# Kernel optimization log

Hardware: AMD Instinct MI355X
Metric: run time of the kernel (lower is better)

## Reference

```python
import jax, jax.numpy as jnp
import numpy as np

BIG_K = 13
EPS = 1e-5  # torch BatchNorm2d default


def setup_inputs() -> dict:
    key = jax.random.key(0)
    k1, k2, k3, k4 = jax.random.split(key, 4)
    B, C1, C2, H, W_ = 8, 256, 256, 64, 64
    x = jax.random.normal(k1, (B, C1, H, W_), dtype=jnp.float32)
    # scale kernel by fan-in so pre-BN activations are O(1)
    fan_in = C1 * BIG_K * BIG_K
    W = jax.random.normal(k2, (C2, C1, BIG_K, BIG_K), dtype=jnp.float32) / np.sqrt(fan_in)
    gamma = jnp.ones((C2,), dtype=jnp.float32)
    beta = jnp.zeros((C2,), dtype=jnp.float32)
    running_mean = jax.random.normal(k3, (C2,), dtype=jnp.float32) * 0.1
    running_var = jax.random.uniform(k4, (C2,), dtype=jnp.float32, minval=0.5, maxval=1.5)
    return {"x": x, "W": W, "gamma": gamma, "beta": beta,
            "running_mean": running_mean, "running_var": running_var}


def reference(x, W, gamma, beta, running_mean, running_var):
    # Fallback path of ShiftWiseConv: big-kernel conv (no bias) -> BN (inference) -> SiLU
    pad = BIG_K // 2
    y = jax.lax.conv_general_dilated(
        x, W,
        window_strides=(1, 1),
        padding=[(pad, pad), (pad, pad)],
        dimension_numbers=("NCHW", "OIHW", "NCHW"),
    )
    inv = gamma * jax.lax.rsqrt(running_var + EPS)  # [C2]
    y = y * inv[None, :, None, None] + (beta - running_mean * inv)[None, :, None, None]
    return jax.nn.silu(y)
```

## Files before the change

kernel.cpp:

```cpp
#include <hip/hip_runtime.h>
#include <stdint.h>

#define EPS 1e-5f

typedef __attribute__((ext_vector_type(8))) __bf16 bf16x8;
typedef __attribute__((ext_vector_type(16))) float f32x16;

__device__ __forceinline__ int swz4(int r) { return (r ^ (r >> 2)) & 3; }

__device__ __forceinline__ unsigned short f2bf(float f) {
  union { float f; unsigned u; } v; v.f = f;
  unsigned r = v.u + 0x7fffu + ((v.u >> 16) & 1u);
  return (unsigned short)(r >> 16);
}

__device__ __forceinline__ void glds16(const unsigned short* g, unsigned short* l) {
  __builtin_amdgcn_global_load_lds(
      (const __attribute__((address_space(1))) void*)g,
      (__attribute__((address_space(3))) void*)l, 16, 0, 0);
}
__device__ __forceinline__ void glds4(const unsigned short* g, unsigned short* l) {
  __builtin_amdgcn_global_load_lds(
      (const __attribute__((address_space(1))) void*)g,
      (__attribute__((address_space(3))) void*)l, 4, 0, 0);
}

template <int N>
__device__ __forceinline__ void vmwait() {
  asm volatile("s_waitcnt vmcnt(%0)" ::"n"(N) : "memory");
}

__global__ __launch_bounds__(256) void pack_w_kernel(
    const float* __restrict__ W, unsigned short* __restrict__ Wp) {
  const int blk = blockIdx.x;
  const int c2 = blk / 13, kh = blk - c2 * 13;
  const int c1 = threadIdx.x;
  const int c2t = c2 >> 7, m = c2 & 127;
  const int c1c = c1 >> 5, c1i = c1 & 31;
  const float* src = W + (((size_t)(c2 * 256 + c1)) * 13 + kh) * 13;
  const int rowoff = (((c1i >> 3) ^ swz4(m)) << 3) + (c1i & 7);
#pragma unroll
  for (int kw = 0; kw < 13; ++kw) {
    const int ks = (kh * 8 + c1c) * 13 + kw;
    const size_t dst = (((size_t)c2t * 1352 + ks) * 128 + m) * 32 + rowoff;
    Wp[dst] = f2bf(src[kw]);
  }
}

__global__ __launch_bounds__(256) void pack_xt_kernel(
    const float* __restrict__ x, unsigned short* __restrict__ xT) {
  const int blk = blockIdx.x;
  const int rowp = blk % 76;
  const int bc = blk / 76;
  const int c1c = bc & 7, b = bc >> 3;
  const int row = rowp - 6;
  const bool rok = (unsigned)row < 64u;
  unsigned short* dst = xT + (size_t)blk * 2560;
  const float* srcb = x + (size_t)(b * 256 + c1c * 32) * 4096 +
                      (rok ? row * 64 : 0);
#pragma unroll
  for (int e = 0; e < 10; ++e) {
    const int idx = e * 256 + threadIdx.x;
    const int colp = idx >> 5, c1i = idx & 31;
    const int ic = colp - 8;
    const float v = (rok && (unsigned)ic < 64u) ? srcb[(size_t)c1i * 4096 + ic] : 0.f;
    dst[colp * 32 + ((((c1i >> 3) ^ swz4(colp)) << 3)) + (c1i & 7)] = f2bf(v);
  }
}

__global__ __launch_bounds__(256, 2) void conv6_kernel(
    const unsigned short* __restrict__ Wp, const unsigned short* __restrict__ xT,
    const float* __restrict__ gamma, const float* __restrict__ beta,
    const float* __restrict__ mean, const float* __restrict__ var,
    float* __restrict__ out) {
  __shared__ __align__(16) unsigned short Abuf[2][8192];
  __shared__ __align__(16) unsigned short Wbuf[2][5120];
  __shared__ float s_scale[128], s_shift[128];

  const int tid = threadIdx.x;
  const int bid = blockIdx.x;
  const int b = bid & 7;
  const int h0 = ((bid >> 3) & 31) * 2;
  const int c2t = bid >> 8;

  const int wid = tid >> 6, lane = tid & 63;
  const int wr = wid >> 1, wc = wid & 1;
  const int l31 = lane & 31, hi2 = lane >> 5;

  if (tid < 128) {
    const int c2 = c2t * 128 + tid;
    const float inv = gamma[c2] * rsqrtf(var[c2] + EPS);
    s_scale[tid] = inv;
    s_shift[tid] = beta[c2] - mean[c2] * inv;
  }

  int aoff[2][2];
#pragma unroll
  for (int mt = 0; mt < 2; ++mt)
#pragma unroll
    for (int ks = 0; ks < 2; ++ks) {
      const int m = wr * 64 + mt * 32 + l31;
      aoff[mt][ks] = m * 64 + (((ks * 2 + hi2) ^ swz4(m)) << 4);
    }
  int ndh[2], nwl[2];
#pragma unroll
  for (int nt = 0; nt < 2; ++nt) {
    const int n = wc * 64 + nt * 32 + l31;
    ndh[nt] = n >> 6;
    nwl[nt] = n & 63;
  }

  const int tid8 = tid * 8, tid2 = tid * 2;
  const int widA = wid * 512, wid128 = wid * 128;

  const size_t c2base = (size_t)c2t * 1352;
  const int bc8 = b * 8;

  auto wtile = [&](int T) -> const unsigned short* {
    const int kh = T >> 3, c1c = T & 7;
    return xT + (size_t)((bc8 + c1c) * 76 + h0 + kh) * 2560;
  };

  f32x16 acc[2][2];
#pragma unroll
  for (int i = 0; i < 2; ++i)
#pragma unroll
    for (int j = 0; j < 2; ++j)
#pragma unroll
      for (int r = 0; r < 16; ++r) acc[i][j][r] = 0.f;

  bf16x8 rA[2][2][2], rB[2][2][2];

  {
    const unsigned short* at0 = Wp + (c2base << 12);
    const unsigned short* at1 = Wp + ((c2base + 1) << 12);
    glds16(at0 + tid8, &Abuf[0][0] + widA);
    glds16(at0 + 2048 + tid8, &Abuf[0][2048] + widA);
    glds16(at1 + tid8, &Abuf[0][4096] + widA);
    glds16(at1 + 2048 + tid8, &Abuf[0][6144] + widA);
    const unsigned short* ws = wtile(0);
    glds16(ws + tid8, &Wbuf[0][0] + widA);
    glds16(ws + 2048 + tid8, &Wbuf[0][2048] + widA);
    glds4(ws + 4096 + tid2, &Wbuf[0][4096] + wid128);
    glds4(ws + 4608 + tid2, &Wbuf[0][4608] + wid128);
    vmwait<0>();
    __builtin_amdgcn_s_barrier();
  }

#define PHASE(PH, KWA, WBA, KWB, WBB, WRT, WSRCP, WDB)                        \
  {                                                                           \
      \
    {                                                                         \
      const char* abA = (const char*)&Abuf[(PH) & 1][0];                      \
      const char* abB = abA + 8192;                                           \
      const char* wbA = (const char*)&Wbuf[(WBA)][0];                         \
      const char* wbB = (const char*)&Wbuf[(WBB)][0];                         \
      _Pragma("unroll") for (int ks = 0; ks < 2; ++ks) {                      \
        rA[0][ks][0] = *(const bf16x8*)(abA + aoff[0][ks]);                   \
        rA[0][ks][1] = *(const bf16x8*)(abA + aoff[1][ks]);                   \
        rA[1][ks][0] = *(const bf16x8*)(abB + aoff[0][ks]);                   \
        rA[1][ks][1] = *(const bf16x8*)(abB + aoff[1][ks]);                   \
        _Pragma("unroll") for (int nt = 0; nt < 2; ++nt) {                    \
          const int colA = nwl[nt] + (KWA) + 2;                               \
          rB[0][ks][nt] = *(const bf16x8*)(                                   \
              wbA + (ndh[nt] * 80 + colA) * 64 +                              \
              (((ks * 2 + hi2) ^ swz4(colA)) << 4));                          \
          const int colB = nwl[nt] + (KWB) + 2;                               \
          rB[1][ks][nt] = *(const bf16x8*)(                                   \
              wbB + (ndh[nt] * 80 + colB) * 64 +                              \
              (((ks * 2 + hi2) ^ swz4(colB)) << 4));                          \
        }                                                                     \
      }                                                                       \
    }                                                                         \
                   \
    {                                                                         \
      int sn0 = S0 + 2 * (PH) + 2;                                            \
      if (sn0 >= 1352) sn0 -= 1352;                                           \
      int sn1 = sn0 + 1;                                                      \
      if (sn1 >= 1352) sn1 -= 1352;                                           \
      const unsigned short* at0 = Wp + ((c2base + (size_t)sn0) << 12);        \
      const unsigned short* at1 = Wp + ((c2base + (size_t)sn1) << 12);        \
      unsigned short* ad = &Abuf[((PH) + 1) & 1][0];                          \
      glds16(at0 + tid8, ad + widA);                                          \
      glds16(at0 + 2048 + tid8, ad + 2048 + widA);                            \
      glds16(at1 + tid8, ad + 4096 + widA);                                   \
      glds16(at1 + 2048 + tid8, ad + 6144 + widA);                            \
    }                                                                         \
    if ((WRT) == 1) glds16((WSRCP) + tid8, &Wbuf[(WDB)][0] + widA);           \
    if ((WRT) == 2)                                                           \
      glds16((WSRCP) + 2048 + tid8, &Wbuf[(WDB)][2048] + widA);               \
    if ((WRT) == 3) {                                                         \
      glds4((WSRCP) + 4096 + tid2, &Wbuf[(WDB)][4096] + wid128);              \
      glds4((WSRCP) + 4608 + tid2, &Wbuf[(WDB)][4608] + wid128);              \
    }                                                                         \
    asm volatile("" ::: "memory");       \
    __builtin_amdgcn_s_barrier();                                             \
    __builtin_amdgcn_sched_barrier(0);              \
           \
    {                                                                         \
      __builtin_amdgcn_s_setprio(1);                                          \
      _Pragma("unroll") for (int s = 0; s < 2; ++s)                           \
          _Pragma("unroll") for (int ks = 0; ks < 2; ++ks) {                  \
        acc[0][0] = __builtin_amdgcn_mfma_f32_32x32x16_bf16(                  \
            rA[s][ks][0], rB[s][ks][0], acc[0][0], 0, 0, 0);                  \
        acc[0][1] = __builtin_amdgcn_mfma_f32_32x32x16_bf16(                  \
            rA[s][ks][0], rB[s][ks][1], acc[0][1], 0, 0, 0);                  \
        acc[1][0] = __builtin_amdgcn_mfma_f32_32x32x16_bf16(                  \
            rA[s][ks][1], rB[s][ks][0], acc[1][0], 0, 0, 0);                  \
        acc[1][1] = __builtin_amdgcn_mfma_f32_32x32x16_bf16(                  \
            rA[s][ks][1], rB[s][ks][1], acc[1][1], 0, 0, 0);                  \
      }                                                                       \
      __builtin_amdgcn_s_setprio(0);                                          \
    }                                                                         \
            \
    vmwait<((WRT) == 0 ? 0 : ((WRT) == 3 ? 2 : 1))>();                        \
    __builtin_amdgcn_s_barrier();                                             \
  }

  for (int u = 0; u < 26; ++u) {
    const int S0 = u * 52;
    const int Tb = u * 4;
    const unsigned short* wt1 = wtile(Tb + 1);
    const unsigned short* wt2 = wtile(Tb + 2);
    const unsigned short* wt3 = wtile(Tb + 3);
    const unsigned short* wt4 = wtile((Tb + 4 == 104) ? 0 : Tb + 4);
    PHASE(0, 0, 0, 1, 0, 0, wt1, 1)
    PHASE(1, 2, 0, 3, 0, 0, wt1, 1)
    PHASE(2, 4, 0, 5, 0, 0, wt1, 1)
    PHASE(3, 6, 0, 7, 0, 1, wt1, 1)
    PHASE(4, 8, 0, 9, 0, 2, wt1, 1)
    PHASE(5, 10, 0, 11, 0, 3, wt1, 1)
    PHASE(6, 12, 0, 0, 1, 0, wt1, 1)
    PHASE(7, 1, 1, 2, 1, 0, wt2, 0)
    PHASE(8, 3, 1, 4, 1, 0, wt2, 0)
    PHASE(9, 5, 1, 6, 1, 1, wt2, 0)
    PHASE(10, 7, 1, 8, 1, 2, wt2, 0)
    PHASE(11, 9, 1, 10, 1, 3, wt2, 0)
    PHASE(12, 11, 1, 12, 1, 0, wt2, 0)
    PHASE(13, 0, 0, 1, 0, 0, wt3, 1)
    PHASE(14, 2, 0, 3, 0, 0, wt3, 1)
    PHASE(15, 4, 0, 5, 0, 0, wt3, 1)
    PHASE(16, 6, 0, 7, 0, 1, wt3, 1)
    PHASE(17, 8, 0, 9, 0, 2, wt3, 1)
    PHASE(18, 10, 0, 11, 0, 3, wt3, 1)
    PHASE(19, 12, 0, 0, 1, 0, wt3, 1)
    PHASE(20, 1, 1, 2, 1, 0, wt4, 0)
    PHASE(21, 3, 1, 4, 1, 0, wt4, 0)
    PHASE(22, 5, 1, 6, 1, 1, wt4, 0)
    PHASE(23, 7, 1, 8, 1, 2, wt4, 0)
    PHASE(24, 9, 1, 10, 1, 3, wt4, 0)
    PHASE(25, 11, 1, 12, 1, 0, wt4, 0)
  }
#undef PHASE

  vmwait<0>();

#pragma unroll
  for (int mt = 0; mt < 2; ++mt) {
#pragma unroll
    for (int nt = 0; nt < 2; ++nt) {
      const int n = wc * 64 + nt * 32 + l31;
      const int hh = h0 + (n >> 6), ww = n & 63;
#pragma unroll
      for (int r = 0; r < 16; ++r) {
        const int mloc = (r & 3) + 8 * (r >> 2) + 4 * hi2;
        const int c2l = wr * 64 + mt * 32 + mloc;
        const float y = acc[mt][nt][r] * s_scale[c2l] + s_shift[c2l];
        out[((size_t)(b * 256 + c2t * 128 + c2l)) * 4096 + hh * 64 + ww] =
            y / (1.f + __expf(-y));
      }
    }
  }
}

__global__ void naive_conv_kernel(
    const float* __restrict__ x, const float* __restrict__ W,
    const float* __restrict__ gamma, const float* __restrict__ beta,
    const float* __restrict__ mean, const float* __restrict__ var,
    float* __restrict__ out) {
  const int idx = blockIdx.x * 256 + threadIdx.x;
  if (idx >= 8 * 256 * 64 * 64) return;
  const int w = idx & 63, h = (idx >> 6) & 63;
  const int c2 = (idx >> 12) & 255, b = idx >> 20;
  float s = 0.f;
  for (int c1 = 0; c1 < 256; ++c1) {
    const float* xp = x + ((size_t)(b * 256 + c1) * 4096);
    const float* wp = W + ((size_t)(c2 * 256 + c1) * 169);
    for (int kh = 0; kh < 13; ++kh) {
      const int r = h + kh - 6;
      if ((unsigned)r >= 64u) continue;
      for (int kw = 0; kw < 13; ++kw) {
        const int c = w + kw - 6;
        if ((unsigned)c >= 64u) continue;
        s += xp[r * 64 + c] * wp[kh * 13 + kw];
      }
    }
  }
  const float inv = gamma[c2] * rsqrtf(var[c2] + EPS);
  const float y = s * inv + (beta[c2] - mean[c2] * inv);
  out[idx] = y / (1.f + __expf(-y));
}

extern "C" void kernel_launch(void* const* d_in, const int* in_sizes, int n_in,
                              void* d_out, int out_size, void* d_ws, size_t ws_size,
                              hipStream_t stream) {
  const float* x = (const float*)d_in[0];
  const float* W = (const float*)d_in[1];
  const float* gamma = (const float*)d_in[2];
  const float* beta = (const float*)d_in[3];
  const float* mean = (const float*)d_in[4];
  const float* var = (const float*)d_in[5];
  float* out = (float*)d_out;

  const size_t WP_BYTES = (size_t)256 * 43264 * 2;
  const size_t XT_BYTES = (size_t)12455424 * 2;

  if (ws_size >= WP_BYTES + XT_BYTES) {
    unsigned short* Wp = (unsigned short*)d_ws;
    unsigned short* xT = (unsigned short*)((char*)d_ws + WP_BYTES);
    pack_w_kernel<<<256 * 13, 256, 0, stream>>>(W, Wp);
    pack_xt_kernel<<<8 * 8 * 76, 256, 0, stream>>>(x, xT);
    conv6_kernel<<<512, 256, 0, stream>>>(Wp, xT, gamma, beta, mean, var, out);
  } else {
    naive_conv_kernel<<<(8 * 256 * 64 * 64 + 255) / 256, 256, 0, stream>>>(
        x, W, gamma, beta, mean, var, out);
  }
}
```

Baseline: 624.0 us.

## Load weight tiles directly from global into registers with double-buffered prefetch

```diff
diff --git a/kernel.cpp b/kernel.cpp
--- a/kernel.cpp
+++ b/kernel.cpp
@@ -38,12 +38,13 @@
   const int c2t = c2 >> 7, m = c2 & 127;
   const int c1c = c1 >> 5, c1i = c1 & 31;
   const float* src = W + (((size_t)(c2 * 256 + c1)) * 13 + kh) * 13;
-  const int rowoff = (((c1i >> 3) ^ swz4(m)) << 3) + (c1i & 7);
+  const int chunk = c1i >> 3, j = c1i & 7;
+  const int intile = (chunk >> 1) * 2048 + (m >> 5) * 512 + (chunk & 1) * 256 +
+                     (m & 31) * 8 + j;
 #pragma unroll
   for (int kw = 0; kw < 13; ++kw) {
     const int ks = (kh * 8 + c1c) * 13 + kw;
-    const size_t dst = (((size_t)c2t * 1352 + ks) * 128 + m) * 32 + rowoff;
-    Wp[dst] = f2bf(src[kw]);
+    Wp[((size_t)c2t * 1352 + ks) * 4096 + intile] = f2bf(src[kw]);
   }
 }
 
@@ -68,12 +69,11 @@
   }
 }
 
-__global__ __launch_bounds__(256, 2) void conv6_kernel(
+__global__ __launch_bounds__(256, 2) void conv7_kernel(
     const unsigned short* __restrict__ Wp, const unsigned short* __restrict__ xT,
     const float* __restrict__ gamma, const float* __restrict__ beta,
     const float* __restrict__ mean, const float* __restrict__ var,
     float* __restrict__ out) {
-  __shared__ __align__(16) unsigned short Abuf[2][8192];
   __shared__ __align__(16) unsigned short Wbuf[2][5120];
   __shared__ float s_scale[128], s_shift[128];
 
@@ -94,14 +94,12 @@
     s_shift[tid] = beta[c2] - mean[c2] * inv;
   }
 
-  int aoff[2][2];
-#pragma unroll
-  for (int mt = 0; mt < 2; ++mt)
-#pragma unroll
-    for (int ks = 0; ks < 2; ++ks) {
-      const int m = wr * 64 + mt * 32 + l31;
-      aoff[mt][ks] = m * 64 + (((ks * 2 + hi2) ^ swz4(m)) << 4);
-    }
+  int offA[2][2];
+#pragma unroll
+  for (int ks = 0; ks < 2; ++ks)
+#pragma unroll
+    for (int mt = 0; mt < 2; ++mt)
+      offA[ks][mt] = ks * 4096 + (wr * 2 + mt) * 1024 + hi2 * 512 + l31 * 16;
   int ndh[2], nwl[2];
 #pragma unroll
   for (int nt = 0; nt < 2; ++nt) {
@@ -115,6 +113,7 @@
 
   const size_t c2base = (size_t)c2t * 1352;
   const int bc8 = b * 8;
+  const char* WpB = (const char*)Wp;
 
   auto wtile = [&](int T) -> const unsigned short* {
     const int kh = T >> 3, c1c = T & 7;
@@ -129,15 +128,9 @@
 #pragma unroll
       for (int r = 0; r < 16; ++r) acc[i][j][r] = 0.f;
 
-  bf16x8 rA[2][2][2], rB[2][2][2];
+  bf16x8 a0[2][2][2], b0[2][2][2], a1[2][2][2], b1[2][2][2];
 
   {
-    const unsigned short* at0 = Wp + (c2base << 12);
-    const unsigned short* at1 = Wp + ((c2base + 1) << 12);
-    glds16(at0 + tid8, &Abuf[0][0] + widA);
-    glds16(at0 + 2048 + tid8, &Abuf[0][2048] + widA);
-    glds16(at1 + tid8, &Abuf[0][4096] + widA);
-    glds16(at1 + 2048 + tid8, &Abuf[0][6144] + widA);
     const unsigned short* ws = wtile(0);
     glds16(ws + tid8, &Wbuf[0][0] + widA);
     glds16(ws + 2048 + tid8, &Wbuf[0][2048] + widA);
@@ -145,47 +138,31 @@
     glds4(ws + 4608 + tid2, &Wbuf[0][4608] + wid128);
     vmwait<0>();
     __builtin_amdgcn_s_barrier();
-  }
-
-#define PHASE(PH, KWA, WBA, KWB, WBB, WRT, WSRCP, WDB)                        \
+    const char* at0 = WpB + (c2base << 13);
+    const char* at1 = WpB + ((c2base + 1) << 13);
+    const char* wb0 = (const char*)&Wbuf[0][0];
+#pragma unroll
+    for (int ks = 0; ks < 2; ++ks)
+#pragma unroll
+      for (int mt = 0; mt < 2; ++mt) {
+        a0[0][ks][mt] = *(const bf16x8*)(at0 + offA[ks][mt]);
+        a0[1][ks][mt] = *(const bf16x8*)(at1 + offA[ks][mt]);
+      }
+#pragma unroll
+    for (int ks = 0; ks < 2; ++ks)
+#pragma unroll
+      for (int nt = 0; nt < 2; ++nt) {
+        const int cA = nwl[nt] + 0 + 2;
+        b0[0][ks][nt] = *(const bf16x8*)(wb0 + (ndh[nt] * 80 + cA) * 64 +
+                                         (((ks * 2 + hi2) ^ swz4(cA)) << 4));
+        const int cB = nwl[nt] + 1 + 2;
+        b0[1][ks][nt] = *(const bf16x8*)(wb0 + (ndh[nt] * 80 + cB) * 64 +
+                                         (((ks * 2 + hi2) ^ swz4(cB)) << 4));
+      }
+  }
+
+#define PHASE(AC, BC, AN, BN, NKWA, NWBA, NKWB, NWBB, SN0E, WRT, WSRCP, WDB)  \
   {                                                                           \
-      \
-    {                                                                         \
-      const char* abA = (const char*)&Abuf[(PH) & 1][0];                      \
-      const char* abB = abA + 8192;                                           \
-      const char* wbA = (const char*)&Wbuf[(WBA)][0];                         \
-      const char* wbB = (const char*)&Wbuf[(WBB)][0];                         \
-      _Pragma("unroll") for (int ks = 0; ks < 2; ++ks) {                      \
-        rA[0][ks][0] = *(const bf16x8*)(abA + aoff[0][ks]);                   \
-        rA[0][ks][1] = *(const bf16x8*)(abA + aoff[1][ks]);                   \
-        rA[1][ks][0] = *(const bf16x8*)(abB + aoff[0][ks]);                   \
-        rA[1][ks][1] = *(const bf16x8*)(abB + aoff[1][ks]);                   \
-        _Pragma("unroll") for (int nt = 0; nt < 2; ++nt) {                    \
-          const int colA = nwl[nt] + (KWA) + 2;                               \
-          rB[0][ks][nt] = *(const bf16x8*)(                                   \
-              wbA + (ndh[nt] * 80 + colA) * 64 +                              \
-              (((ks * 2 + hi2) ^ swz4(colA)) << 4));                          \
-          const int colB = nwl[nt] + (KWB) + 2;                               \
-          rB[1][ks][nt] = *(const bf16x8*)(                                   \
-              wbB + (ndh[nt] * 80 + colB) * 64 +                              \
-              (((ks * 2 + hi2) ^ swz4(colB)) << 4));                          \
-        }                                                                     \
-      }                                                                       \
-    }                                                                         \
-                   \
-    {                                                                         \
-      int sn0 = S0 + 2 * (PH) + 2;                                            \
-      if (sn0 >= 1352) sn0 -= 1352;                                           \
-      int sn1 = sn0 + 1;                                                      \
-      if (sn1 >= 1352) sn1 -= 1352;                                           \
-      const unsigned short* at0 = Wp + ((c2base + (size_t)sn0) << 12);        \
-      const unsigned short* at1 = Wp + ((c2base + (size_t)sn1) << 12);        \
-      unsigned short* ad = &Abuf[((PH) + 1) & 1][0];                          \
-      glds16(at0 + tid8, ad + widA);                                          \
-      glds16(at0 + 2048 + tid8, ad + 2048 + widA);                            \
-      glds16(at1 + tid8, ad + 4096 + widA);                                   \
-      glds16(at1 + 2048 + tid8, ad + 6144 + widA);                            \
-    }                                                                         \
     if ((WRT) == 1) glds16((WSRCP) + tid8, &Wbuf[(WDB)][0] + widA);           \
     if ((WRT) == 2)                                                           \
       glds16((WSRCP) + 2048 + tid8, &Wbuf[(WDB)][2048] + widA);               \
@@ -193,28 +170,50 @@
       glds4((WSRCP) + 4096 + tid2, &Wbuf[(WDB)][4096] + wid128);              \
       glds4((WSRCP) + 4608 + tid2, &Wbuf[(WDB)][4608] + wid128);              \
     }                                                                         \
-    asm volatile("" ::: "memory");       \
-    __builtin_amdgcn_s_barrier();                                             \
-    __builtin_amdgcn_sched_barrier(0);              \
-           \
+    {                                                                         \
+      int sn0 = (SN0E);                                                       \
+      if (sn0 >= 1352) sn0 -= 1352;                                           \
+      const char* at0 = WpB + ((c2base + (size_t)sn0) << 13);                 \
+      const char* at1 = at0 + 8192;                                           \
+      _Pragma("unroll") for (int ks = 0; ks < 2; ++ks)                        \
+          _Pragma("unroll") for (int mt = 0; mt < 2; ++mt) {                  \
+        AN[0][ks][mt] = *(const bf16x8*)(at0 + offA[ks][mt]);                 \
+        AN[1][ks][mt] = *(const bf16x8*)(at1 + offA[ks][mt]);                 \
+      }                                                                       \
+    }                                                                         \
+    {                                                                         \
+      const char* wbA = (const char*)&Wbuf[(NWBA)][0];                        \
+      const char* wbB = (const char*)&Wbuf[(NWBB)][0];                        \
+      _Pragma("unroll") for (int ks = 0; ks < 2; ++ks)                        \
+          _Pragma("unroll") for (int nt = 0; nt < 2; ++nt) {                  \
+        const int cA = nwl[nt] + (NKWA) + 2;                                  \
+        BN[0][ks][nt] = *(const bf16x8*)(                                     \
+            wbA + (ndh[nt] * 80 + cA) * 64 +                                  \
+            (((ks * 2 + hi2) ^ swz4(cA)) << 4));                              \
+        const int cB = nwl[nt] + (NKWB) + 2;                                  \
+        BN[1][ks][nt] = *(const bf16x8*)(                                     \
+            wbB + (ndh[nt] * 80 + cB) * 64 +                                  \
+            (((ks * 2 + hi2) ^ swz4(cB)) << 4));                              \
+      }                                                                       \
+    }                                                                         \
     {                                                                         \
       __builtin_amdgcn_s_setprio(1);                                          \
       _Pragma("unroll") for (int s = 0; s < 2; ++s)                           \
           _Pragma("unroll") for (int ks = 0; ks < 2; ++ks) {                  \
         acc[0][0] = __builtin_amdgcn_mfma_f32_32x32x16_bf16(                  \
-            rA[s][ks][0], rB[s][ks][0], acc[0][0], 0, 0, 0);                  \
+            AC[s][ks][0], BC[s][ks][0], acc[0][0], 0, 0, 0);                  \
         acc[0][1] = __builtin_amdgcn_mfma_f32_32x32x16_bf16(                  \
-            rA[s][ks][0], rB[s][ks][1], acc[0][1], 0, 0, 0);                  \
+            AC[s][ks][0], BC[s][ks][1], acc[0][1], 0, 0, 0);                  \
         acc[1][0] = __builtin_amdgcn_mfma_f32_32x32x16_bf16(                  \
-            rA[s][ks][1], rB[s][ks][0], acc[1][0], 0, 0, 0);                  \
+            AC[s][ks][1], BC[s][ks][0], acc[1][0], 0, 0, 0);                  \
         acc[1][1] = __builtin_amdgcn_mfma_f32_32x32x16_bf16(                  \
-            rA[s][ks][1], rB[s][ks][1], acc[1][1], 0, 0, 0);                  \
+            AC[s][ks][1], BC[s][ks][1], acc[1][1], 0, 0, 0);                  \
       }                                                                       \
       __builtin_amdgcn_s_setprio(0);                                          \
     }                                                                         \
-            \
-    vmwait<((WRT) == 0 ? 0 : ((WRT) == 3 ? 2 : 1))>();                        \
+    vmwait<6>();                                                              \
     __builtin_amdgcn_s_barrier();                                             \
+    __builtin_amdgcn_sched_barrier(0);                                        \
   }
 
   for (int u = 0; u < 26; ++u) {
@@ -224,32 +223,32 @@
     const unsigned short* wt2 = wtile(Tb + 2);
     const unsigned short* wt3 = wtile(Tb + 3);
     const unsigned short* wt4 = wtile((Tb + 4 == 104) ? 0 : Tb + 4);
-    PHASE(0, 0, 0, 1, 0, 0, wt1, 1)
-    PHASE(1, 2, 0, 3, 0, 0, wt1, 1)
-    PHASE(2, 4, 0, 5, 0, 0, wt1, 1)
-    PHASE(3, 6, 0, 7, 0, 1, wt1, 1)
-    PHASE(4, 8, 0, 9, 0, 2, wt1, 1)
-    PHASE(5, 10, 0, 11, 0, 3, wt1, 1)
-    PHASE(6, 12, 0, 0, 1, 0, wt1, 1)
-    PHASE(7, 1, 1, 2, 1, 0, wt2, 0)
-    PHASE(8, 3, 1, 4, 1, 0, wt2, 0)
-    PHASE(9, 5, 1, 6, 1, 1, wt2, 0)
-    PHASE(10, 7, 1, 8, 1, 2, wt2, 0)
-    PHASE(11, 9, 1, 10, 1, 3, wt2, 0)
-    PHASE(12, 11, 1, 12, 1, 0, wt2, 0)
-    PHASE(13, 0, 0, 1, 0, 0, wt3, 1)
-    PHASE(14, 2, 0, 3, 0, 0, wt3, 1)
-    PHASE(15, 4, 0, 5, 0, 0, wt3, 1)
-    PHASE(16, 6, 0, 7, 0, 1, wt3, 1)
-    PHASE(17, 8, 0, 9, 0, 2, wt3, 1)
-    PHASE(18, 10, 0, 11, 0, 3, wt3, 1)
-    PHASE(19, 12, 0, 0, 1, 0, wt3, 1)
-    PHASE(20, 1, 1, 2, 1, 0, wt4, 0)
-    PHASE(21, 3, 1, 4, 1, 0, wt4, 0)
-    PHASE(22, 5, 1, 6, 1, 1, wt4, 0)
-    PHASE(23, 7, 1, 8, 1, 2, wt4, 0)
-    PHASE(24, 9, 1, 10, 1, 3, wt4, 0)
-    PHASE(25, 11, 1, 12, 1, 0, wt4, 0)
+    PHASE(a0, b0, a1, b1, 2, 0, 3, 0, S0 + 2, 0, wt1, 1)
+    PHASE(a1, b1, a0, b0, 4, 0, 5, 0, S0 + 4, 1, wt1, 1)
+    PHASE(a0, b0, a1, b1, 6, 0, 7, 0, S0 + 6, 2, wt1, 1)
+    PHASE(a1, b1, a0, b0, 8, 0, 9, 0, S0 + 8, 3, wt1, 1)
+    PHASE(a0, b0, a1, b1, 10, 0, 11, 0, S0 + 10, 0, wt1, 1)
+    PHASE(a1, b1, a0, b0, 12, 0, 0, 1, S0 + 12, 0, wt1, 1)
+    PHASE(a0, b0, a1, b1, 1, 1, 2, 1, S0 + 14, 0, wt1, 1)
+    PHASE(a1, b1, a0, b0, 3, 1, 4, 1, S0 + 16, 0, wt2, 0)
+    PHASE(a0, b0, a1, b1, 5, 1, 6, 1, S0 + 18, 1, wt2, 0)
+    PHASE(a1, b1, a0, b0, 7, 1, 8, 1, S0 + 20, 2, wt2, 0)
+    PHASE(a0, b0, a1, b1, 9, 1, 10, 1, S0 + 22, 3, wt2, 0)
+    PHASE(a1, b1, a0, b0, 11, 1, 12, 1, S0 + 24, 0, wt2, 0)
+    PHASE(a0, b0, a1, b1, 0, 0, 1, 0, S0 + 26, 0, wt2, 0)
+    PHASE(a1, b1, a0, b0, 2, 0, 3, 0, S0 + 28, 0, wt3, 1)
+    PHASE(a0, b0, a1, b1, 4, 0, 5, 0, S0 + 30, 1, wt3, 1)
+    PHASE(a1, b1, a0, b0, 6, 0, 7, 0, S0 + 32, 2, wt3, 1)
+    PHASE(a0, b0, a1, b1, 8, 0, 9, 0, S0 + 34, 3, wt3, 1)
+    PHASE(a1, b1, a0, b0, 10, 0, 11, 0, S0 + 36, 0, wt3, 1)
+    PHASE(a0, b0, a1, b1, 12, 0, 0, 1, S0 + 38, 0, wt3, 1)
+    PHASE(a1, b1, a0, b0, 1, 1, 2, 1, S0 + 40, 0, wt3, 1)
+    PHASE(a0, b0, a1, b1, 3, 1, 4, 1, S0 + 42, 0, wt4, 0)
+    PHASE(a1, b1, a0, b0, 5, 1, 6, 1, S0 + 44, 1, wt4, 0)
+    PHASE(a0, b0, a1, b1, 7, 1, 8, 1, S0 + 46, 2, wt4, 0)
+    PHASE(a1, b1, a0, b0, 9, 1, 10, 1, S0 + 48, 3, wt4, 0)
+    PHASE(a0, b0, a1, b1, 11, 1, 12, 1, S0 + 50, 0, wt4, 0)
+    PHASE(a1, b1, a0, b0, 0, 0, 1, 0, S0 + 52, 0, wt4, 0)
   }
 #undef PHASE
 
@@ -320,7 +319,7 @@
     unsigned short* xT = (unsigned short*)((char*)d_ws + WP_BYTES);
     pack_w_kernel<<<256 * 13, 256, 0, stream>>>(W, Wp);
     pack_xt_kernel<<<8 * 8 * 76, 256, 0, stream>>>(x, xT);
-    conv6_kernel<<<512, 256, 0, stream>>>(Wp, xT, gamma, beta, mean, var, out);
+    conv7_kernel<<<512, 256, 0, stream>>>(Wp, xT, gamma, beta, mean, var, out);
   } else {
     naive_conv_kernel<<<(8 * 256 * 64 * 64 + 255) / 256, 256, 0, stream>>>(
         x, W, gamma, beta, mean, var, out);
```

New measurement: 753.3 us. 20.7% more time.

## Triple-buffer weight tiles in LDS to prefetch two phases ahead

Applied to the files above, without the earlier changes.

```diff
diff --git a/kernel.cpp b/kernel.cpp
--- a/kernel.cpp
+++ b/kernel.cpp
@@ -68,12 +68,12 @@
   }
 }
 
-__global__ __launch_bounds__(256, 2) void conv6_kernel(
+__global__ __launch_bounds__(256, 2) void conv10_kernel(
     const unsigned short* __restrict__ Wp, const unsigned short* __restrict__ xT,
     const float* __restrict__ gamma, const float* __restrict__ beta,
     const float* __restrict__ mean, const float* __restrict__ var,
     float* __restrict__ out) {
-  __shared__ __align__(16) unsigned short Abuf[2][8192];
+  __shared__ __align__(16) unsigned short Abuf[3][8192];
   __shared__ __align__(16) unsigned short Wbuf[2][5120];
   __shared__ float s_scale[128], s_shift[128];
 
@@ -94,13 +94,13 @@
     s_shift[tid] = beta[c2] - mean[c2] * inv;
   }
 
-  int aoff[2][2];
+  int aoffs[2][2];
 #pragma unroll
   for (int mt = 0; mt < 2; ++mt)
 #pragma unroll
     for (int ks = 0; ks < 2; ++ks) {
       const int m = wr * 64 + mt * 32 + l31;
-      aoff[mt][ks] = m * 64 + (((ks * 2 + hi2) ^ swz4(m)) << 4);
+      aoffs[mt][ks] = m * 64 + (((ks * 2 + hi2) ^ swz4(m)) << 4);
     }
   int ndh[2], nwl[2];
 #pragma unroll
@@ -115,6 +115,8 @@
 
   const size_t c2base = (size_t)c2t * 1352;
   const int bc8 = b * 8;
+  const char* Abase = (const char*)&Abuf[0][0];
+  unsigned short* AbaseU = &Abuf[0][0];
 
   auto wtile = [&](int T) -> const unsigned short* {
     const int kh = T >> 3, c1c = T & 7;
@@ -131,35 +133,45 @@
 
   bf16x8 rA[2][2][2], rB[2][2][2];
 
+  int aRd = 0, aMid = 16384, aWr = 32768;
+
   {
     const unsigned short* at0 = Wp + (c2base << 12);
     const unsigned short* at1 = Wp + ((c2base + 1) << 12);
-    glds16(at0 + tid8, &Abuf[0][0] + widA);
-    glds16(at0 + 2048 + tid8, &Abuf[0][2048] + widA);
-    glds16(at1 + tid8, &Abuf[0][4096] + widA);
-    glds16(at1 + 2048 + tid8, &Abuf[0][6144] + widA);
+    glds16(at0 + tid8, AbaseU + widA);
+    glds16(at0 + 2048 + tid8, AbaseU + 2048 + widA);
+    glds16(at1 + tid8, AbaseU + 4096 + widA);
+    glds16(at1 + 2048 + tid8, AbaseU + 6144 + widA);
     const unsigned short* ws = wtile(0);
     glds16(ws + tid8, &Wbuf[0][0] + widA);
     glds16(ws + 2048 + tid8, &Wbuf[0][2048] + widA);
     glds4(ws + 4096 + tid2, &Wbuf[0][4096] + wid128);
     glds4(ws + 4608 + tid2, &Wbuf[0][4608] + wid128);
-    vmwait<0>();
+    const unsigned short* at2 = Wp + ((c2base + 2) << 12);
+    const unsigned short* at3 = Wp + ((c2base + 3) << 12);
+    unsigned short* ad1 = AbaseU + 8192;
+    glds16(at2 + tid8, ad1 + widA);
+    glds16(at2 + 2048 + tid8, ad1 + 2048 + widA);
+    glds16(at3 + tid8, ad1 + 4096 + widA);
+    glds16(at3 + 2048 + tid8, ad1 + 6144 + widA);
+    vmwait<4>();
     __builtin_amdgcn_s_barrier();
+    __builtin_amdgcn_sched_barrier(0);
   }
 
 #define PHASE(PH, KWA, WBA, KWB, WBB, WRT, WSRCP, WDB)                        \
   {                                                                           \
-      \
+        \
     {                                                                         \
-      const char* abA = (const char*)&Abuf[(PH) & 1][0];                      \
+      const char* abA = Abase + aRd;                                          \
       const char* abB = abA + 8192;                                           \
       const char* wbA = (const char*)&Wbuf[(WBA)][0];                         \
       const char* wbB = (const char*)&Wbuf[(WBB)][0];                         \
       _Pragma("unroll") for (int ks = 0; ks < 2; ++ks) {                      \
-        rA[0][ks][0] = *(const bf16x8*)(abA + aoff[0][ks]);                   \
-        rA[0][ks][1] = *(const bf16x8*)(abA + aoff[1][ks]);                   \
-        rA[1][ks][0] = *(const bf16x8*)(abB + aoff[0][ks]);                   \
-        rA[1][ks][1] = *(const bf16x8*)(abB + aoff[1][ks]);                   \
+        rA[0][ks][0] = *(const bf16x8*)(abA + aoffs[0][ks]);                  \
+        rA[0][ks][1] = *(const bf16x8*)(abA + aoffs[1][ks]);                  \
+        rA[1][ks][0] = *(const bf16x8*)(abB + aoffs[0][ks]);                  \
+        rA[1][ks][1] = *(const bf16x8*)(abB + aoffs[1][ks]);                  \
         _Pragma("unroll") for (int nt = 0; nt < 2; ++nt) {                    \
           const int colA = nwl[nt] + (KWA) + 2;                               \
           rB[0][ks][nt] = *(const bf16x8*)(                                   \
@@ -172,20 +184,7 @@
         }                                                                     \
       }                                                                       \
     }                                                                         \
-                   \
-    {                                                                         \
-      int sn0 = S0 + 2 * (PH) + 2;                                            \
-      if (sn0 >= 1352) sn0 -= 1352;                                           \
-      int sn1 = sn0 + 1;                                                      \
-      if (sn1 >= 1352) sn1 -= 1352;                                           \
-      const unsigned short* at0 = Wp + ((c2base + (size_t)sn0) << 12);        \
-      const unsigned short* at1 = Wp + ((c2base + (size_t)sn1) << 12);        \
-      unsigned short* ad = &Abuf[((PH) + 1) & 1][0];                          \
-      glds16(at0 + tid8, ad + widA);                                          \
-      glds16(at0 + 2048 + tid8, ad + 2048 + widA);                            \
-      glds16(at1 + tid8, ad + 4096 + widA);                                   \
-      glds16(at1 + 2048 + tid8, ad + 6144 + widA);                            \
-    }                                                                         \
+                                              \
     if ((WRT) == 1) glds16((WSRCP) + tid8, &Wbuf[(WDB)][0] + widA);           \
     if ((WRT) == 2)                                                           \
       glds16((WSRCP) + 2048 + tid8, &Wbuf[(WDB)][2048] + widA);               \
@@ -193,10 +192,24 @@
       glds4((WSRCP) + 4096 + tid2, &Wbuf[(WDB)][4096] + wid128);              \
       glds4((WSRCP) + 4608 + tid2, &Wbuf[(WDB)][4608] + wid128);              \
     }                                                                         \
-    asm volatile("" ::: "memory");       \
+        \
+    {                                                                         \
+      int sn0 = S0 + 2 * (PH) + 4;                                            \
+      if (sn0 >= 1352) sn0 -= 1352;                                           \
+      int sn1 = sn0 + 1;                                                      \
+      if (sn1 >= 1352) sn1 -= 1352;                                           \
+      const unsigned short* at0 = Wp + ((c2base + (size_t)sn0) << 12);        \
+      const unsigned short* at1 = Wp + ((c2base + (size_t)sn1) << 12);        \
+      unsigned short* ad = AbaseU + (aWr >> 1);                               \
+      glds16(at0 + tid8, ad + widA);                                          \
+      glds16(at0 + 2048 + tid8, ad + 2048 + widA);                            \
+      glds16(at1 + tid8, ad + 4096 + widA);                                   \
+      glds16(at1 + 2048 + tid8, ad + 6144 + widA);                            \
+    }                                                                         \
+    asm volatile("" ::: "memory");                                            \
     __builtin_amdgcn_s_barrier();                                             \
-    __builtin_amdgcn_sched_barrier(0);              \
-           \
+    __builtin_amdgcn_sched_barrier(0);                                        \
+                                         \
     {                                                                         \
       __builtin_amdgcn_s_setprio(1);                                          \
       _Pragma("unroll") for (int s = 0; s < 2; ++s)                           \
@@ -212,9 +225,10 @@
       }                                                                       \
       __builtin_amdgcn_s_setprio(0);                                          \
     }                                                                         \
-            \
-    vmwait<((WRT) == 0 ? 0 : ((WRT) == 3 ? 2 : 1))>();                        \
+             \
+    vmwait<((WRT) == 0 ? 4 : ((WRT) == 3 ? 6 : 5))>();                        \
     __builtin_amdgcn_s_barrier();                                             \
+    { const int t_ = aRd; aRd = aMid; aMid = aWr; aWr = t_; }                 \
   }
 
   for (int u = 0; u < 26; ++u) {
@@ -320,7 +334,7 @@
     unsigned short* xT = (unsigned short*)((char*)d_ws + WP_BYTES);
     pack_w_kernel<<<256 * 13, 256, 0, stream>>>(W, Wp);
     pack_xt_kernel<<<8 * 8 * 76, 256, 0, stream>>>(x, xT);
-    conv6_kernel<<<512, 256, 0, stream>>>(Wp, xT, gamma, beta, mean, var, out);
+    conv10_kernel<<<512, 256, 0, stream>>>(Wp, xT, gamma, beta, mean, var, out);
   } else {
     naive_conv_kernel<<<(8 * 256 * 64 * 64 + 255) / 256, 256, 0, stream>>>(
         x, W, gamma, beta, mean, var, out);
```

Measured after the change: 615.2 us. No clear change (-1.4%).
